# Optimization experiments

Measured on AMD Instinct MI355X. Metric: run time of the kernel, lower is better.

The kernel has to match this reference:

```python
import jax, jax.numpy as jnp
import numpy as np

B, S, D, H = 2, 2048, 1024, 16
DK = D // H

def setup_inputs() -> dict:
    key = jax.random.key(0)
    ks = jax.random.split(key, 12)
    scale = 1.0 / np.sqrt(D)
    inp = {
        'q': jax.random.normal(ks[0], (B, S, D), jnp.float32),
        'k': jax.random.normal(ks[1], (B, S, D), jnp.float32),
        'v': jax.random.normal(ks[2], (B, S, D), jnp.float32),
        # causal mask: 1 where attending is allowed (j <= i), 0 for future tokens
        'mask': jnp.tril(jnp.ones((S, S), jnp.int32))[None, None, :, :],
        'wq': jax.random.normal(ks[3], (D, D), jnp.float32) * scale,
        'bq': jnp.zeros((D,), jnp.float32),
        'wk': jax.random.normal(ks[4], (D, D), jnp.float32) * scale,
        'bk': jnp.zeros((D,), jnp.float32),
        'wv': jax.random.normal(ks[5], (D, D), jnp.float32) * scale,
        'bv': jnp.zeros((D,), jnp.float32),
        'wo': jax.random.normal(ks[6], (D, D), jnp.float32) * scale,
        'bo': jnp.zeros((D,), jnp.float32),
    }
    return inp


def reference(q, k, v, mask, wq, bq, wk, bk, wv, bv, wo, bo):
    def split_heads(x):
        # [B,S,D] -> [B,H,S,DK]
        return x.reshape(B, S, H, DK).transpose(0, 2, 1, 3)

    query = split_heads(q @ wq + bq)
    key_ = split_heads(k @ wk + bk)
    value = split_heads(v @ wv + bv)

    # [B,H,S,S] attention scores
    scores = jnp.einsum('bhqd,bhkd->bhqk', query, key_) / jnp.sqrt(
        jnp.asarray(DK, jnp.float32))
    scores = jnp.where(mask == 0, jnp.asarray(-1e9, scores.dtype), scores)
    attn = jax.nn.softmax(scores, axis=-1)  # dropout p=0.0 (eval mode)

    x = jnp.einsum('bhqk,bhkd->bhqd', attn, value)  # [B,H,S,DK]
    x = x.transpose(0, 2, 1, 3).reshape(B, S, D)
    return x @ wo + bo
```

## Files before the change

### kernel.cpp

```cpp
#include <hip/hip_runtime.h>
#include <hip/hip_bf16.h>

#define BATCH 2
#define SEQ   2048
#define DMODEL 1024
#define NHEAD 16
#define DK    64
#define MTOK  (BATCH * SEQ)

typedef __attribute__((ext_vector_type(8))) short bf16x8;
typedef __attribute__((ext_vector_type(4))) float f32x4;

__device__ __forceinline__ unsigned short f2bf(float x) {
    unsigned u = __float_as_uint(x);
    u = (u + 0x7FFFu + ((u >> 16) & 1u)) >> 16;
    return (unsigned short)u;
}

__device__ __forceinline__ void store_out(float* p, float v)          { *p = v; }
__device__ __forceinline__ void store_out(unsigned short* p, float v) { *p = f2bf(v); }

__device__ __forceinline__ void g2lds16(const void* g, void* l) {
    __builtin_amdgcn_global_load_lds(
        (const __attribute__((address_space(1))) void*)g,
        (__attribute__((address_space(3))) void*)l, 16, 0, 0);
}

template <int N>
__device__ __forceinline__ void s_wait_vmcnt() {
    asm volatile("s_waitcnt vmcnt(%0)" :: "n"(N) : "memory");
}
__device__ __forceinline__ void s_wait_lgkm0() {
    asm volatile("s_waitcnt lgkmcnt(0)" ::: "memory");
}
__device__ __forceinline__ void s_bar() {
    asm volatile("s_barrier" ::: "memory");
}

__global__ __launch_bounds__(256) void cvt3_bf16_kernel(
    const float* __restrict__ s0, const float* __restrict__ s1,
    const float* __restrict__ s2,
    unsigned short* __restrict__ d0, unsigned short* __restrict__ d1,
    unsigned short* __restrict__ d2, int n)
{
    const float* src; unsigned short* dst;
    switch (blockIdx.z) {
        case 0:  src = s0; dst = d0; break;
        case 1:  src = s1; dst = d1; break;
        default: src = s2; dst = d2; break;
    }
    int i = (blockIdx.x * 256 + threadIdx.x) * 8;
    if (i >= n) return;
    float4 a = *(const float4*)(src + i);
    float4 b = *(const float4*)(src + i + 4);
    union { unsigned short s[8]; uint4 u; } o;
    o.s[0] = f2bf(a.x); o.s[1] = f2bf(a.y); o.s[2] = f2bf(a.z); o.s[3] = f2bf(a.w);
    o.s[4] = f2bf(b.x); o.s[5] = f2bf(b.y); o.s[6] = f2bf(b.z); o.s[7] = f2bf(b.w);
    *(uint4*)(dst + i) = o.u;
}

__global__ __launch_bounds__(256) void wtrans_kernel(
    const float* __restrict__ w0, const float* __restrict__ w1,
    const float* __restrict__ w2, const float* __restrict__ w3,
    unsigned short* __restrict__ t0, unsigned short* __restrict__ t1,
    unsigned short* __restrict__ t2, unsigned short* __restrict__ t3)
{
    __shared__ float tile[32][33];
    const float* W; unsigned short* T;
    switch (blockIdx.z) {
        case 0:  W = w0; T = t0; break;
        case 1:  W = w1; T = t1; break;
        case 2:  W = w2; T = t2; break;
        default: W = w3; T = t3; break;
    }
    const int n0 = blockIdx.x * 32, k0 = blockIdx.y * 32;
    const int t  = threadIdx.x;
    const int r  = t >> 3;
    const int c4 = (t & 7) * 4;

    float4 v = *(const float4*)&W[(size_t)(k0 + r) * DMODEL + n0 + c4];
    tile[r][c4 + 0] = v.x; tile[r][c4 + 1] = v.y;
    tile[r][c4 + 2] = v.z; tile[r][c4 + 3] = v.w;
    __syncthreads();

    union { unsigned short s[4]; uint2 u; } o;
#pragma unroll
    for (int u = 0; u < 4; ++u) o.s[u] = f2bf(tile[c4 + u][r]);
    *(uint2*)&T[(size_t)(n0 + r) * DMODEL + k0 + c4] = o.u;
}

struct GemmP {
    const unsigned short* A;
    const unsigned short* Bt;
    const float* bias;
    void* C;
    int N, K, ctShift, biasByRow;
    float scale;
};
struct Gemm3 { GemmP p[3]; };

template <typename OutT, int NTILE>
__global__ __launch_bounds__(256) void gemm_lds_kernel(Gemm3 g)
{
    constexpr int NBLK  = 16 + 4 * NTILE;
    constexpr int BUFSZ = NBLK * 512;
    constexpr int PW    = NBLK / 4;

    __shared__ unsigned short sS[2][BUFSZ];

    const GemmP p = g.p[blockIdx.z];
    const unsigned short* __restrict__ A  = p.A;
    const unsigned short* __restrict__ Bt = p.Bt;
    OutT* __restrict__ C = (OutT*)p.C;
    const int K = p.K, N = p.N;

    const int bid = blockIdx.x;
    const int bx = bid & ((1 << p.ctShift) - 1);
    const int by = bid >> p.ctShift;
    const int row0 = by * 128;
    const int col0 = bx * (NTILE * 32);

    const int t    = threadIdx.x;
    const int w    = t >> 6;
    const int lane = t & 63;
    const int ln   = lane & 15;
    const int qg   = lane >> 4;
    const int wm   = w >> 1;
    const int wn   = w & 1;

    const unsigned short* sp[PW];
    unsigned short* lp[PW];
#pragma unroll
    for (int i = 0; i < PW; ++i) {
        const int s = w * PW + i;
        if (s < 16) {
            const int mtg = s >> 1, kc = s & 1;
            sp[i] = A + (size_t)(row0 + mtg * 16 + ln) * K + kc * 32 + qg * 8;
        } else {
            const int bi = s - 16;
            const int ntg = bi >> 1, kc = bi & 1;
            sp[i] = Bt + (size_t)(col0 + ntg * 16 + ln) * K + kc * 32 + qg * 8;
        }
        lp[i] = &sS[0][s * 512];
    }

    f32x4 acc[4][NTILE];
#pragma unroll
    for (int mt = 0; mt < 4; ++mt)
#pragma unroll
        for (int nt = 0; nt < NTILE; ++nt) acc[mt][nt] = (f32x4){0.f, 0.f, 0.f, 0.f};

    const int nt = K / 64;

#pragma unroll
    for (int i = 0; i < PW; ++i) g2lds16(sp[i], lp[i]);
    if (nt > 1) {
#pragma unroll
        for (int i = 0; i < PW; ++i) g2lds16(sp[i] + 64, lp[i] + BUFSZ);
    }

    int cur = 0;
    for (int kt = 0; kt < nt; ++kt) {
        if (kt < nt - 1) s_wait_vmcnt<PW>();
        else             s_wait_vmcnt<0>();
        s_bar();

        const unsigned short* bufA = &sS[cur][0];
        const unsigned short* bufB = &sS[cur][16 * 512];
#pragma unroll
        for (int kc = 0; kc < 2; ++kc) {
            bf16x8 aF[4], bF[NTILE];
#pragma unroll
            for (int mt = 0; mt < 4; ++mt)
                aF[mt] = *(const bf16x8*)&bufA[(((wm * 4 + mt) * 2) + kc) * 512 + lane * 8];
#pragma unroll
            for (int n2 = 0; n2 < NTILE; ++n2)
                bF[n2] = *(const bf16x8*)&bufB[(((wn * NTILE + n2) * 2) + kc) * 512 + lane * 8];
#pragma unroll
            for (int mt = 0; mt < 4; ++mt)
#pragma unroll
                for (int n2 = 0; n2 < NTILE; ++n2)
                    acc[mt][n2] = __builtin_amdgcn_mfma_f32_16x16x32_bf16(
                        aF[mt], bF[n2], acc[mt][n2], 0, 0, 0);
        }

        s_wait_lgkm0();
        s_bar();

        if (kt + 2 < nt) {
            const int koff = (kt + 2) * 64;
#pragma unroll
            for (int i = 0; i < PW; ++i)
                g2lds16(sp[i] + koff, lp[i] + cur * BUFSZ);
        }
        cur ^= 1;
    }

    float bcol[NTILE], brow[4][4];
    if (!p.biasByRow) {
#pragma unroll
        for (int n2 = 0; n2 < NTILE; ++n2)
            bcol[n2] = p.bias[col0 + wn * NTILE * 16 + n2 * 16 + ln];
    } else {
#pragma unroll
        for (int mt = 0; mt < 4; ++mt)
#pragma unroll
            for (int r = 0; r < 4; ++r)
                brow[mt][r] = p.bias[row0 + wm * 64 + mt * 16 + qg * 4 + r];
    }

#pragma unroll
    for (int mt = 0; mt < 4; ++mt)
#pragma unroll
        for (int n2 = 0; n2 < NTILE; ++n2)
#pragma unroll
            for (int r = 0; r < 4; ++r) {
                int row = row0 + wm * 64 + mt * 16 + qg * 4 + r;
                int col = col0 + wn * NTILE * 16 + n2 * 16 + ln;
                float bb = p.biasByRow ? brow[mt][r] : bcol[n2];
                store_out(&C[(size_t)row * N + col], (acc[mt][n2][r] + bb) * p.scale);
            }
}

#define BR 64
#define BC 64
#define PSTR 72

__global__ __launch_bounds__(256) void attn_mfma_kernel(
    const unsigned short* __restrict__ Qg, const unsigned short* __restrict__ Kg,
    const unsigned short* __restrict__ VT, unsigned short* __restrict__ O)
{
    __shared__ unsigned short sK[2][8 * 512];
    __shared__ unsigned short sV[2][8 * 512];
    __shared__ unsigned short sQ[8 * 512];
    __shared__ unsigned short sP[BR * PSTR];

    const int t    = threadIdx.x;
    const int w    = t >> 6;
    const int lane = t & 63;
    const int ln   = lane & 15;
    const int qg   = lane >> 4;

    const int id  = blockIdx.x;
    const int bh  = id & 31;
    const int qt  = (SEQ / BR - 1) - (id >> 5);
    const int b   = bh >> 4;
    const int h   = bh & 15;
    const int qi0 = qt * BR;

    const size_t rowbase = (size_t)b * SEQ;
    const size_t colbase = (size_t)h * DK;

#pragma unroll
    for (int i = 0; i < 2; ++i) {
        const int s = w * 2 + i;
        const int nt = s >> 1, kc = s & 1;
        g2lds16(Qg + (rowbase + qi0 + w * 16 + ln) * DMODEL + colbase + i * 32 + qg * 8,
                &sQ[s * 512]);
        g2lds16(Kg + (rowbase + nt * 16 + ln) * DMODEL + colbase + kc * 32 + qg * 8,
                &sK[0][s * 512]);
        g2lds16(VT + (size_t)(colbase + nt * 16 + ln) * MTOK + rowbase + kc * 32 + qg * 8,
                &sV[0][s * 512]);
    }
    __syncthreads();

    bf16x8 aq[2];
#pragma unroll
    for (int kc = 0; kc < 2; ++kc)
        aq[kc] = *(const bf16x8*)&sQ[(w * 2 + kc) * 512 + lane * 8];

    const short one_bf = (short)0x3F80;
    const bf16x8 bone = (bf16x8){one_bf, one_bf, one_bf, one_bf,
                                 one_bf, one_bf, one_bf, one_bf};

    f32x4 ofrag[4];
#pragma unroll
    for (int nt = 0; nt < 4; ++nt) ofrag[nt] = (f32x4){0.f, 0.f, 0.f, 0.f};
    f32x4 osum = (f32x4){0.f, 0.f, 0.f, 0.f};
    float m_r[4];
#pragma unroll
    for (int r = 0; r < 4; ++r) m_r[r] = -3.0e38f;

    const int ntiles = qt + 1;
    for (int jt = 0; jt < ntiles; ++jt) {
        const int cur = jt & 1;

        if (jt + 1 < ntiles) {
            const int j1 = (jt + 1) * BC;
            const int nb = cur ^ 1;
#pragma unroll
            for (int i = 0; i < 2; ++i) {
                const int s = w * 2 + i;
                const int nt = s >> 1, kc = s & 1;
                g2lds16(Kg + (rowbase + j1 + nt * 16 + ln) * DMODEL + colbase + kc * 32 + qg * 8,
                        &sK[nb][s * 512]);
                g2lds16(VT + (size_t)(colbase + nt * 16 + ln) * MTOK + rowbase + j1 + kc * 32 + qg * 8,
                        &sV[nb][s * 512]);
            }
        }

        f32x4 sf[4];
#pragma unroll
        for (int nt = 0; nt < 4; ++nt) {
            f32x4 a2 = (f32x4){0.f, 0.f, 0.f, 0.f};
#pragma unroll
            for (int kc = 0; kc < 2; ++kc) {
                bf16x8 bk = *(const bf16x8*)&sK[cur][(nt * 2 + kc) * 512 + lane * 8];
                a2 = __builtin_amdgcn_mfma_f32_16x16x32_bf16(aq[kc], bk, a2, 0, 0, 0);
            }
            sf[nt] = a2;
        }

        if (jt == ntiles - 1) {
#pragma unroll
            for (int nt = 0; nt < 4; ++nt)
#pragma unroll
                for (int r = 0; r < 4; ++r) {
                    int qrow = w * 16 + qg * 4 + r;
                    int col  = nt * 16 + ln;
                    if (col > qrow) sf[nt][r] = -1.0e30f;
                }
        }

        float rmax[4];
#pragma unroll
        for (int r = 0; r < 4; ++r)
            rmax[r] = fmaxf(fmaxf(sf[0][r], sf[1][r]), fmaxf(sf[2][r], sf[3][r]));
#pragma unroll
        for (int off = 8; off >= 1; off >>= 1)
#pragma unroll
            for (int r = 0; r < 4; ++r)
                rmax[r] = fmaxf(rmax[r], __shfl_xor(rmax[r], off));

        float alpha[4];
#pragma unroll
        for (int r = 0; r < 4; ++r) {
            float mn = fmaxf(m_r[r], rmax[r]);
            alpha[r] = exp2f(m_r[r] - mn);
            m_r[r] = mn;
        }

#pragma unroll
        for (int nt = 0; nt < 4; ++nt)
#pragma unroll
            for (int r = 0; r < 4; ++r) {
                float pv = exp2f(sf[nt][r] - m_r[r]);
                int row = w * 16 + qg * 4 + r;
                int col = (nt * 16 + ln) ^ (((w * 4 + qg) & 7) * 8);
                sP[row * PSTR + col] = f2bf(pv);
            }

#pragma unroll
        for (int nt = 0; nt < 4; ++nt)
#pragma unroll
            for (int r = 0; r < 4; ++r) ofrag[nt][r] *= alpha[r];
#pragma unroll
        for (int r = 0; r < 4; ++r) osum[r] *= alpha[r];

        bf16x8 apf[2];
#pragma unroll
        for (int kc = 0; kc < 2; ++kc) {
            int row = w * 16 + ln;
            int col = (kc * 32 + qg * 8) ^ ((((row >> 2) & 7)) * 8);
            apf[kc] = *(const bf16x8*)&sP[row * PSTR + col];
        }

#pragma unroll
        for (int kc = 0; kc < 2; ++kc)
            osum = __builtin_amdgcn_mfma_f32_16x16x32_bf16(apf[kc], bone, osum, 0, 0, 0);
#pragma unroll
        for (int nt = 0; nt < 4; ++nt) {
#pragma unroll
            for (int kc = 0; kc < 2; ++kc) {
                bf16x8 bv = *(const bf16x8*)&sV[cur][(nt * 2 + kc) * 512 + lane * 8];
                ofrag[nt] = __builtin_amdgcn_mfma_f32_16x16x32_bf16(apf[kc], bv, ofrag[nt], 0, 0, 0);
            }
        }

        __syncthreads();
    }

    float inv[4];
#pragma unroll
    for (int r = 0; r < 4; ++r) inv[r] = 1.0f / osum[r];
#pragma unroll
    for (int nt = 0; nt < 4; ++nt)
#pragma unroll
        for (int r = 0; r < 4; ++r) {
            int gq = qi0 + w * 16 + qg * 4 + r;
            O[(rowbase + gq) * DMODEL + colbase + nt * 16 + ln] =
                f2bf(ofrag[nt][r] * inv[r]);
        }
}

extern "C" void kernel_launch(void* const* d_in, const int* in_sizes, int n_in,
                              void* d_out, int out_size, void* d_ws, size_t ws_size,
                              hipStream_t stream)
{
    const float* q  = (const float*)d_in[0];
    const float* k  = (const float*)d_in[1];
    const float* v  = (const float*)d_in[2];
    const float* wq = (const float*)d_in[4];
    const float* bq = (const float*)d_in[5];
    const float* wk = (const float*)d_in[6];
    const float* bk = (const float*)d_in[7];
    const float* wv = (const float*)d_in[8];
    const float* bv = (const float*)d_in[9];
    const float* wo = (const float*)d_in[10];
    const float* bo = (const float*)d_in[11];
    float* out = (float*)d_out;

    const size_t mat  = (size_t)MTOK * DMODEL;
    const size_t wmat = (size_t)DMODEL * DMODEL;
    unsigned short* Abq = (unsigned short*)d_ws;
    unsigned short* Abk = Abq + mat;
    unsigned short* Abv = Abk + mat;
    unsigned short* WtQ = Abv + mat;
    unsigned short* WtK = WtQ + wmat;
    unsigned short* WtV = WtK + wmat;
    unsigned short* WtO = WtV + wmat;
    unsigned short* Qb  = WtO + wmat;
    unsigned short* Kb  = Qb + mat;
    unsigned short* VT  = Kb + mat;
    unsigned short* CTX = VT + mat;

    cvt3_bf16_kernel<<<dim3((unsigned)(mat / 2048), 1, 3), 256, 0, stream>>>(
        q, k, v, Abq, Abk, Abv, (int)mat);
    wtrans_kernel<<<dim3(32, 32, 4), 256, 0, stream>>>(wq, wk, wv, wo, WtQ, WtK, WtV, WtO);

    const float qscale = 0.125f * 1.44269504088896f;
    Gemm3 g;
    g.p[0] = (GemmP){Abq, WtQ, bq, (void*)Qb, DMODEL, DMODEL, 3, 0, qscale};
    g.p[1] = (GemmP){Abk, WtK, bk, (void*)Kb, DMODEL, DMODEL, 3, 0, 1.0f};
    g.p[2] = (GemmP){WtV, Abv, bv, (void*)VT, MTOK,   DMODEL, 5, 1, 1.0f};
    gemm_lds_kernel<unsigned short, 4><<<dim3(256, 1, 3), 256, 0, stream>>>(g);

    attn_mfma_kernel<<<BATCH * NHEAD * (SEQ / BR), 256, 0, stream>>>(Qb, Kb, VT, CTX);

    Gemm3 go;
    go.p[0] = (GemmP){CTX, WtO, bo, (void*)out, DMODEL, DMODEL, 4, 0, 1.0f};
    go.p[1] = go.p[0];
    go.p[2] = go.p[0];
    gemm_lds_kernel<float, 2><<<dim3(512, 1, 1), 256, 0, stream>>>(go);
}
```

Before: 258.6 us.

## Enlarge GEMM tiles to 256 rows with 8 waves and XCD-aware block remap

Result: slower. 270.4 us (+4.5%).

```diff
diff --git a/kernel.cpp b/kernel.cpp
--- a/kernel.cpp
+++ b/kernel.cpp
@@ -99,87 +99,92 @@
 };
 struct Gemm3 { GemmP p[3]; };
 
-template <typename OutT, int NTILE>
-__global__ __launch_bounds__(256) void gemm_lds_kernel(Gemm3 g)
+template <typename OutT, int NC>
+__global__ __launch_bounds__(512, 2) void gemm_lds_kernel(Gemm3 g)
 {
-    constexpr int NBLK  = 16 + 4 * NTILE;
+    constexpr int NCW   = NC / 4;
+    constexpr int NBLK  = 32 + 2 * NC;
+    constexpr int PW    = NBLK / 8;
     constexpr int BUFSZ = NBLK * 512;
-    constexpr int PW    = NBLK / 4;
-
-    __shared__ unsigned short sS[2][BUFSZ];
-
-    const GemmP p = g.p[blockIdx.z];
+
+    __shared__ unsigned short sS[2 * BUFSZ];
+
+    const unsigned nx  = gridDim.x;
+    const unsigned lin = blockIdx.x + nx * blockIdx.z;
+    const unsigned ch  = (nx * gridDim.z) >> 3;
+    const unsigned l2  = (lin & 7u) * ch + (lin >> 3);
+    const unsigned zz  = l2 / nx;
+    const unsigned bid = l2 - zz * nx;
+
+    const GemmP p = g.p[zz];
     const unsigned short* __restrict__ A  = p.A;
     const unsigned short* __restrict__ Bt = p.Bt;
     OutT* __restrict__ C = (OutT*)p.C;
     const int K = p.K, N = p.N;
 
-    const int bid = blockIdx.x;
-    const int bx = bid & ((1 << p.ctShift) - 1);
-    const int by = bid >> p.ctShift;
-    const int row0 = by * 128;
-    const int col0 = bx * (NTILE * 32);
+    const int bx = (int)(bid & ((1u << p.ctShift) - 1u));
+    const int by = (int)(bid >> p.ctShift);
+    const int row0 = by * 256;
+    const int col0 = bx * (NC * 16);
 
     const int t    = threadIdx.x;
     const int w    = t >> 6;
     const int lane = t & 63;
     const int ln   = lane & 15;
     const int qg   = lane >> 4;
-    const int wm   = w >> 1;
-    const int wn   = w & 1;
+    const int wm   = w >> 2;
+    const int wn   = w & 3;
 
     const unsigned short* sp[PW];
-    unsigned short* lp[PW];
+    int lo[PW];
 #pragma unroll
     for (int i = 0; i < PW; ++i) {
         const int s = w * PW + i;
-        if (s < 16) {
+        if (s < 32) {
             const int mtg = s >> 1, kc = s & 1;
             sp[i] = A + (size_t)(row0 + mtg * 16 + ln) * K + kc * 32 + qg * 8;
         } else {
-            const int bi = s - 16;
+            const int bi = s - 32;
             const int ntg = bi >> 1, kc = bi & 1;
             sp[i] = Bt + (size_t)(col0 + ntg * 16 + ln) * K + kc * 32 + qg * 8;
         }
-        lp[i] = &sS[0][s * 512];
-    }
-
-    f32x4 acc[4][NTILE];
-#pragma unroll
-    for (int mt = 0; mt < 4; ++mt)
-#pragma unroll
-        for (int nt = 0; nt < NTILE; ++nt) acc[mt][nt] = (f32x4){0.f, 0.f, 0.f, 0.f};
-
-    const int nt = K / 64;
-
-#pragma unroll
-    for (int i = 0; i < PW; ++i) g2lds16(sp[i], lp[i]);
-    if (nt > 1) {
-#pragma unroll
-        for (int i = 0; i < PW; ++i) g2lds16(sp[i] + 64, lp[i] + BUFSZ);
-    }
-
-    int cur = 0;
-    for (int kt = 0; kt < nt; ++kt) {
-        if (kt < nt - 1) s_wait_vmcnt<PW>();
+        lo[i] = s * 512;
+    }
+
+    f32x4 acc[8][NCW];
+#pragma unroll
+    for (int mt = 0; mt < 8; ++mt)
+#pragma unroll
+        for (int nt = 0; nt < NCW; ++nt) acc[mt][nt] = (f32x4){0.f, 0.f, 0.f, 0.f};
+
+    const int NT = K / 64;
+
+#pragma unroll
+    for (int i = 0; i < PW; ++i) g2lds16(sp[i], &sS[lo[i]]);
+#pragma unroll
+    for (int i = 0; i < PW; ++i) g2lds16(sp[i] + 64, &sS[BUFSZ + lo[i]]);
+
+    int curOff = 0;
+    for (int kt = 0; kt < NT; ++kt) {
+        if (kt < NT - 1) s_wait_vmcnt<PW>();
         else             s_wait_vmcnt<0>();
         s_bar();
 
-        const unsigned short* bufA = &sS[cur][0];
-        const unsigned short* bufB = &sS[cur][16 * 512];
+        const unsigned short* bufA = &sS[curOff];
+        const unsigned short* bufB = &sS[curOff + 32 * 512];
 #pragma unroll
         for (int kc = 0; kc < 2; ++kc) {
-            bf16x8 aF[4], bF[NTILE];
-#pragma unroll
-            for (int mt = 0; mt < 4; ++mt)
-                aF[mt] = *(const bf16x8*)&bufA[(((wm * 4 + mt) * 2) + kc) * 512 + lane * 8];
-#pragma unroll
-            for (int n2 = 0; n2 < NTILE; ++n2)
-                bF[n2] = *(const bf16x8*)&bufB[(((wn * NTILE + n2) * 2) + kc) * 512 + lane * 8];
-#pragma unroll
-            for (int mt = 0; mt < 4; ++mt)
-#pragma unroll
-                for (int n2 = 0; n2 < NTILE; ++n2)
+            bf16x8 aF[8], bF[NCW];
+#pragma unroll
+            for (int mt = 0; mt < 8; ++mt)
+                aF[mt] = *(const bf16x8*)&bufA[(((wm * 8 + mt) * 2) + kc) * 512 + lane * 8];
+#pragma unroll
+            for (int n2 = 0; n2 < NCW; ++n2)
+                bF[n2] = *(const bf16x8*)&bufB[(((wn * NCW + n2) * 2) + kc) * 512 + lane * 8];
+#pragma unroll
+            for (int mt = 0; mt < 8; ++mt)
+#pragma unroll
+                for (int n2 = 0; n2 < NCW; ++n2)
                     acc[mt][n2] = __builtin_amdgcn_mfma_f32_16x16x32_bf16(
                         aF[mt], bF[n2], acc[mt][n2], 0, 0, 0);
         }
@@ -187,36 +192,36 @@
         s_wait_lgkm0();
         s_bar();
 
-        if (kt + 2 < nt) {
+        if (kt + 2 < NT) {
             const int koff = (kt + 2) * 64;
 #pragma unroll
             for (int i = 0; i < PW; ++i)
-                g2lds16(sp[i] + koff, lp[i] + cur * BUFSZ);
-        }
-        cur ^= 1;
-    }
-
-    float bcol[NTILE], brow[4][4];
+                g2lds16(sp[i] + koff, &sS[curOff + lo[i]]);
+        }
+        curOff ^= BUFSZ;
+    }
+
+    float bcol[NCW], brow[8][4];
     if (!p.biasByRow) {
 #pragma unroll
-        for (int n2 = 0; n2 < NTILE; ++n2)
-            bcol[n2] = p.bias[col0 + wn * NTILE * 16 + n2 * 16 + ln];
+        for (int n2 = 0; n2 < NCW; ++n2)
+            bcol[n2] = p.bias[col0 + (wn * NCW + n2) * 16 + ln];
     } else {
 #pragma unroll
-        for (int mt = 0; mt < 4; ++mt)
+        for (int mt = 0; mt < 8; ++mt)
 #pragma unroll
             for (int r = 0; r < 4; ++r)
-                brow[mt][r] = p.bias[row0 + wm * 64 + mt * 16 + qg * 4 + r];
-    }
-
-#pragma unroll
-    for (int mt = 0; mt < 4; ++mt)
-#pragma unroll
-        for (int n2 = 0; n2 < NTILE; ++n2)
+                brow[mt][r] = p.bias[row0 + wm * 128 + mt * 16 + qg * 4 + r];
+    }
+
+#pragma unroll
+    for (int mt = 0; mt < 8; ++mt)
+#pragma unroll
+        for (int n2 = 0; n2 < NCW; ++n2)
 #pragma unroll
             for (int r = 0; r < 4; ++r) {
-                int row = row0 + wm * 64 + mt * 16 + qg * 4 + r;
-                int col = col0 + wn * NTILE * 16 + n2 * 16 + ln;
+                int row = row0 + wm * 128 + mt * 16 + qg * 4 + r;
+                int col = col0 + (wn * NCW + n2) * 16 + ln;
                 float bb = p.biasByRow ? brow[mt][r] : bcol[n2];
                 store_out(&C[(size_t)row * N + col], (acc[mt][n2][r] + bb) * p.scale);
             }
@@ -430,16 +435,16 @@
 
     const float qscale = 0.125f * 1.44269504088896f;
     Gemm3 g;
-    g.p[0] = (GemmP){Abq, WtQ, bq, (void*)Qb, DMODEL, DMODEL, 3, 0, qscale};
-    g.p[1] = (GemmP){Abk, WtK, bk, (void*)Kb, DMODEL, DMODEL, 3, 0, 1.0f};
-    g.p[2] = (GemmP){WtV, Abv, bv, (void*)VT, MTOK,   DMODEL, 5, 1, 1.0f};
-    gemm_lds_kernel<unsigned short, 4><<<dim3(256, 1, 3), 256, 0, stream>>>(g);
+    g.p[0] = (GemmP){Abq, WtQ, bq, (void*)Qb, DMODEL, DMODEL, 2, 0, qscale};
+    g.p[1] = (GemmP){Abk, WtK, bk, (void*)Kb, DMODEL, DMODEL, 2, 0, 1.0f};
+    g.p[2] = (GemmP){WtV, Abv, bv, (void*)VT, MTOK,   DMODEL, 4, 1, 1.0f};
+    gemm_lds_kernel<unsigned short, 16><<<dim3(64, 1, 3), 512, 0, stream>>>(g);
 
     attn_mfma_kernel<<<BATCH * NHEAD * (SEQ / BR), 256, 0, stream>>>(Qb, Kb, VT, CTX);
 
     Gemm3 go;
-    go.p[0] = (GemmP){CTX, WtO, bo, (void*)out, DMODEL, DMODEL, 4, 0, 1.0f};
+    go.p[0] = (GemmP){CTX, WtO, bo, (void*)out, DMODEL, DMODEL, 3, 0, 1.0f};
     go.p[1] = go.p[0];
     go.p[2] = go.p[0];
-    gemm_lds_kernel<float, 2><<<dim3(512, 1, 1), 256, 0, stream>>>(go);
-}
+    gemm_lds_kernel<float, 8><<<dim3(128, 1, 1), 512, 0, stream>>>(go);
+}
```
